# Optimization experiments

Hardware: AMD Instinct MI355X
Metric: run time of the kernel (lower is better)

The kernel has to match this reference:

```python
import jax, jax.numpy as jnp
import numpy as np

DIM = 1024


def setup_inputs() -> dict:
    key = jax.random.key(0)
    kx, kw = jax.random.split(key)
    x = jax.random.normal(kx, (4, 2048, DIM), dtype=jnp.float32)
    # fused qkv projection weight, torch Linear convention: [out_features, in_features]
    W_qkv = jax.random.normal(kw, (3 * DIM, DIM), dtype=jnp.float32) * (DIM ** -0.5)
    return {"x": x, "W_qkv": W_qkv}


def reference(x, W_qkv):
    # fused QKV projection: y = x @ W^T -> [B, N, 3*DIM]
    qkv = jnp.einsum('bnd,ed->bne', x, W_qkv)
    B, N, _ = qkv.shape
    # rearrange 'b n (e d) -> e b n d' with e=3
    qkv = qkv.reshape(B, N, 3, DIM).transpose(2, 0, 1, 3)
    q, k, v = qkv[0], qkv[1], qkv[2]
    scale = DIM ** (-0.5)  # note: scale uses full dim, module never splits heads
    attn = jnp.einsum('bnd,bmd->bnm', q * scale, k)  # [B, N, N]
    attn = jax.nn.softmax(attn, axis=-1)
    out = jnp.einsum('bnm,bmd->bnd', attn, v)
    return out
```

## Files before the change

kernel.cpp:

```cpp
#include <hip/hip_runtime.h>

using half8   = __attribute__((ext_vector_type(8))) _Float16;
using f32x4   = __attribute__((ext_vector_type(4))) float;
using ushort8 = __attribute__((ext_vector_type(8))) unsigned short;

__device__ __forceinline__ void gload16(const void* g, void* l) {
  __builtin_amdgcn_global_load_lds(
      (const __attribute__((address_space(1))) void*)g,
      (__attribute__((address_space(3))) void*)l, 16, 0, 0);
}

__device__ __forceinline__ void xcd_swizzle(int& x, int& y, int& z) {
  const int gx = gridDim.x, gy = gridDim.y;
  const int nwg = gx * gy * gridDim.z;
  const int f = blockIdx.x + gx * (blockIdx.y + gy * blockIdx.z);
  const int w = (f & 7) * (nwg >> 3) + (f >> 3);
  const int r = w >> 5, u = w & 31;
  const int nrx = gx >> 3, nry = gy >> 2;
  const int pz  = nrx * nry;
  const int rz  = r / pz, rr = r % pz;
  x = (rr % nrx) * 8 + (u & 7);
  y = (rr / nrx) * 4 + (u >> 3);
  z = rz;
}

__global__ __launch_bounds__(256) void cast_f32_f16(
    const float* __restrict__ in, unsigned short* __restrict__ out, long n) {
  long i = ((long)blockIdx.x * 256 + threadIdx.x) * 8;
  if (i >= n) return;
  float4 a = *(const float4*)(in + i);
  float4 b = *(const float4*)(in + i + 4);
  union { _Float16 h[8]; ushort8 u; } r;
  r.h[0] = (_Float16)a.x; r.h[1] = (_Float16)a.y;
  r.h[2] = (_Float16)a.z; r.h[3] = (_Float16)a.w;
  r.h[4] = (_Float16)b.x; r.h[5] = (_Float16)b.y;
  r.h[6] = (_Float16)b.z; r.h[7] = (_Float16)b.w;
  *(ushort8*)(out + i) = r.u;
}

#define FENCE_N()                                                                  \
  do {                                                                             \
    if constexpr (N_REP == 2)      asm volatile("s_waitcnt vmcnt(2)" ::: "memory");\
    else if constexpr (N_REP == 3) asm volatile("s_waitcnt vmcnt(3)" ::: "memory");\
    else                           asm volatile("s_waitcnt vmcnt(4)" ::: "memory");\
  } while (0)

#define PHASE(P, AC, AN, BC, BNX)                                                  \
  {                                                                                \
    __builtin_amdgcn_s_barrier();                                                  \
    asm volatile("s_waitcnt lgkmcnt(0)" ::: "memory");                             \
    __builtin_amdgcn_sched_barrier(0);                                             \
    __builtin_amdgcn_s_setprio(1);                                                 \
    _Pragma("unroll") for (int ks = 0; ks < 2; ++ks)                               \
    _Pragma("unroll") for (int i = 0; i < 2; ++i)                                  \
    _Pragma("unroll") for (int ni = 0; ni < N_REP; ++ni)                           \
      acc[2 * (P) + i][ni] = __builtin_amdgcn_mfma_f32_16x16x32_f16(               \
          AC[i][ks], BC[ni][ks], acc[2 * (P) + i][ni], 0, 0, 0);                   \
    __builtin_amdgcn_s_setprio(0);                                                 \
    __builtin_amdgcn_sched_barrier(0);                                             \
    if ((P) == 0 && t + 1 < nt) {                                                  \
      unsigned short* d = ldsA + (SLOT ^ 1) * ASZ + wv * 512;                      \
      const long kt = (long)(t + 1) * 64;                                          \
      gload16(aS + kt, d);                                                         \
      gload16(aS + (long)64 * lda + kt, d + 4096);                                 \
      gload16(aS + (long)128 * lda + kt, d + 8192);                                \
      gload16(aS + (long)192 * lda + kt, d + 12288);                               \
    }                                                                              \
    if ((P) == 1 && t + 2 < nt) {                                                  \
      const long kt = (long)(t + 2) * 64;                                          \
      _Pragma("unroll") for (int j = 0; j < N_REP; ++j)                            \
        gload16(bS + (long)(j * 64) * ldb + kt,                                    \
                ldsB + SLOT * BSZ + j * 4096 + wv * 512);                          \
    }                                                                              \
    if ((P) < 3) {                                                                 \
      _Pragma("unroll") for (int i = 0; i < 2; ++i) {                              \
        AN[i][0] = *(const half8*)(lA + aRd + (2 * ((P) + 1) + i) * 2048 + kg0);   \
        AN[i][1] = *(const half8*)(lA + aRd + (2 * ((P) + 1) + i) * 2048 + kg1);   \
      }                                                                            \
    } else if (t + 1 < nt) {                                                       \
      _Pragma("unroll") for (int i = 0; i < 2; ++i) {                              \
        AN[i][0] = *(const half8*)(lAo + aRd + i * 2048 + kg0);                    \
        AN[i][1] = *(const half8*)(lAo + aRd + i * 2048 + kg1);                    \
      }                                                                            \
      _Pragma("unroll") for (int ni = 0; ni < N_REP; ++ni) {                       \
        BNX[ni][0] = *(const half8*)(lBo + bRd + ni * 2048 + kg0);                 \
        BNX[ni][1] = *(const half8*)(lBo + bRd + ni * 2048 + kg1);                 \
      }                                                                            \
    }                                                                              \
    if ((P) == 2) {                                                                \
      if (t + 2 < nt) FENCE_N();                                                   \
      else asm volatile("s_waitcnt vmcnt(0)" ::: "memory");                        \
    }                                                                              \
    __builtin_amdgcn_sched_barrier(0);                                             \
  }

#define TILE(T, S, BCARR, BNARR)                                                   \
  {                                                                                \
    const int t = (T);                                                             \
    constexpr int SLOT = (S);                                                      \
    const char* lA  = (const char*)(ldsA + SLOT * ASZ);                            \
    const char* lAo = (const char*)(ldsA + (SLOT ^ 1) * ASZ);                      \
    const char* lBo = (const char*)(ldsB + (SLOT ^ 1) * BSZ);                      \
    PHASE(0, afE, afO, BCARR, BNARR)                                               \
    PHASE(1, afO, afE, BCARR, BNARR)                                               \
    PHASE(2, afE, afO, BCARR, BNARR)                                               \
    PHASE(3, afO, afE, BCARR, BNARR)                                               \
  }

template <int MODE, int N_REP>
__global__ __launch_bounds__(512, 2) void gemm8p(
    const unsigned short* __restrict__ Ab, const unsigned short* __restrict__ Bb,
    int K, int lda, int ldb, long sA, long sB,
    void* __restrict__ o0, void* __restrict__ o1, void* __restrict__ o2) {
  constexpr int BM  = 256;
  constexpr int BN  = 64 * N_REP;
  constexpr int ASZ = BM * 64;
  constexpr int BSZ = BN * 64;
  __shared__ unsigned short lds[2 * ASZ + 2 * BSZ];

  const int tid  = threadIdx.x;
  const int lane = tid & 63;
  const int wv   = tid >> 6;
  const int wr   = wv >> 2, wc = wv & 3;
  const int fr   = lane & 15, fq = lane >> 4;
  int bxi, byi, bzi;
  xcd_swizzle(bxi, byi, bzi);
  const int bm = byi * BM;
  const int bn = bxi * BN;
  const int bz = bzi;

  const unsigned short* A = Ab + (long)bz * sA;
  const unsigned short* B = Bb + (long)bz * sB;

  const int row_s = tid >> 3;
  const int col_s = ((tid & 7) ^ (row_s & 7)) * 8;
  const unsigned short* aS = A + (long)(bm + row_s) * lda + col_s;
  const unsigned short* bS = B + (long)(bn + row_s) * ldb + col_s;
  unsigned short* ldsA = lds;
  unsigned short* ldsB = lds + 2 * ASZ;

  const int kg0 = ((0 * 4 + fq) ^ (fr & 7)) * 16;
  const int kg1 = ((1 * 4 + fq) ^ (fr & 7)) * 16;
  const int aRd = (wr * 128 + fr) * 128;
  const int bRd = (wc * (16 * N_REP) + fr) * 128;

  f32x4 acc[8][N_REP] = {};
  half8 afE[2][2], afO[2][2];
  half8 bf0[N_REP][2], bf1[N_REP][2];

  const int nt = K / 64;

#pragma unroll
  for (int i = 0; i < 4; ++i)
    gload16(aS + (long)(i * 64) * lda, ldsA + i * 4096 + wv * 512);
#pragma unroll
  for (int j = 0; j < N_REP; ++j)
    gload16(bS + (long)(j * 64) * ldb, ldsB + j * 4096 + wv * 512);
  asm volatile("s_waitcnt vmcnt(0)" ::: "memory");
  __builtin_amdgcn_s_barrier();
  {
    const char* lA0 = (const char*)ldsA;
    const char* lB0 = (const char*)ldsB;
#pragma unroll
    for (int i = 0; i < 2; ++i) {
      afE[i][0] = *(const half8*)(lA0 + aRd + i * 2048 + kg0);
      afE[i][1] = *(const half8*)(lA0 + aRd + i * 2048 + kg1);
    }
#pragma unroll
    for (int ni = 0; ni < N_REP; ++ni) {
      bf0[ni][0] = *(const half8*)(lB0 + bRd + ni * 2048 + kg0);
      bf0[ni][1] = *(const half8*)(lB0 + bRd + ni * 2048 + kg1);
    }
  }
#pragma unroll
  for (int j = 0; j < N_REP; ++j)
    gload16(bS + (long)(j * 64) * ldb + 64, ldsB + BSZ + j * 4096 + wv * 512);

  for (int tt = 0; tt < nt; tt += 2) {
    TILE(tt, 0, bf0, bf1)
    TILE(tt + 1, 1, bf1, bf0)
  }

  const int row0 = bm + wr * 128 + fq * 4;
  const int col0 = bn + wc * (16 * N_REP) + fr;
#pragma unroll
  for (int mi = 0; mi < 8; ++mi) {
#pragma unroll
    for (int ni = 0; ni < N_REP; ++ni) {
      f32x4 c = acc[mi][ni];
      const long r0 = row0 + mi * 16;
      const long e  = col0 + ni * 16;
      if constexpr (MODE == 0) {
        _Float16* q  = (_Float16*)o0;
        _Float16* kk = (_Float16*)o1;
        _Float16* vv = (_Float16*)o2;
#pragma unroll
        for (int j = 0; j < 4; ++j) {
          const long i = r0 + j;
          const float val = c[j];
          if (e < 1024)      q [i * 1024 + e]          = (_Float16)(val * 0.03125f);
          else if (e < 2048) kk[i * 1024 + (e - 1024)] = (_Float16)val;
          else               vv[i * 1024 + (e - 2048)] = (_Float16)val;
        }
      } else if constexpr (MODE == 1) {
        float* C = (float*)o0 + (long)bz * 2048 * 2048;
#pragma unroll
        for (int j = 0; j < 4; ++j) C[(r0 + j) * 2048 + e] = c[j];
      } else {
        float* C = (float*)o0 + (long)bz * 2048 * 1024;
#pragma unroll
        for (int j = 0; j < 4; ++j) C[(r0 + j) * 1024 + e] = c[j];
      }
    }
  }
}

__global__ __launch_bounds__(256) void transpose_v(
    const unsigned short* __restrict__ v, unsigned short* __restrict__ vT) {
  __shared__ unsigned short t[64][72];
  const long b = blockIdx.z;
  const unsigned short* vb = v + b * (2048L * 1024);
  unsigned short* ob = vT + b * (1024L * 2048);
  const int n0 = blockIdx.y * 64;
  const int d0 = blockIdx.x * 64;
  const int tid = threadIdx.x;
  const int r  = tid >> 2;
  const int c0 = (tid & 3) * 16;
  const unsigned short* src = vb + (long)(n0 + r) * 1024 + d0 + c0;
  *(ushort4*)&t[r][c0]      = *(const ushort4*)(src);
  *(ushort4*)&t[r][c0 + 4]  = *(const ushort4*)(src + 4);
  *(ushort4*)&t[r][c0 + 8]  = *(const ushort4*)(src + 8);
  *(ushort4*)&t[r][c0 + 12] = *(const ushort4*)(src + 12);
  __syncthreads();
  union { unsigned short h[8]; ushort8 u; } w0, w1;
#pragma unroll
  for (int j = 0; j < 8; ++j) w0.h[j] = t[c0 + j][r];
#pragma unroll
  for (int j = 0; j < 8; ++j) w1.h[j] = t[c0 + 8 + j][r];
  unsigned short* dst = ob + (long)(d0 + r) * 2048 + n0 + c0;
  *(ushort8*)dst       = w0.u;
  *(ushort8*)(dst + 8) = w1.u;
}

__global__ __launch_bounds__(256) void softmax_rows(float* __restrict__ S) {
  const long row = blockIdx.x;
  float* p = S + row * 2048;
  const int t = threadIdx.x;
  float4 v0 = *(const float4*)(p + t * 8);
  float4 v1 = *(const float4*)(p + t * 8 + 4);
  float f[8] = {v0.x, v0.y, v0.z, v0.w, v1.x, v1.y, v1.z, v1.w};
  float m = f[0];
#pragma unroll
  for (int j = 1; j < 8; ++j) m = fmaxf(m, f[j]);
  for (int o = 32; o; o >>= 1) m = fmaxf(m, __shfl_xor(m, o));
  __shared__ float redm[4];
  if (!(t & 63)) redm[t >> 6] = m;
  __syncthreads();
  m = fmaxf(fmaxf(redm[0], redm[1]), fmaxf(redm[2], redm[3]));
  float e[8], s = 0.f;
#pragma unroll
  for (int j = 0; j < 8; ++j) { e[j] = __expf(f[j] - m); s += e[j]; }
  for (int o = 32; o; o >>= 1) s += __shfl_xor(s, o);
  __shared__ float reds[4];
  if (!(t & 63)) reds[t >> 6] = s;
  __syncthreads();
  s = reds[0] + reds[1] + reds[2] + reds[3];
  const float inv = 1.0f / s;
  union { _Float16 h[8]; ushort8 u; } r;
#pragma unroll
  for (int j = 0; j < 8; ++j) r.h[j] = (_Float16)(e[j] * inv);
  *(ushort8*)((unsigned short*)p + t * 8) = r.u;
}

extern "C" void kernel_launch(void* const* d_in, const int* in_sizes, int n_in,
                              void* d_out, int out_size, void* d_ws, size_t ws_size,
                              hipStream_t stream) {
  const float* x = (const float*)d_in[0];
  const float* W = (const float*)d_in[1];
  float* out = (float*)d_out;
  char* ws = (char*)d_ws;

  const long MB16 = 16777216;
  unsigned short* q  = (unsigned short*)(ws);
  unsigned short* k  = (unsigned short*)(ws + MB16);
  unsigned short* vT = (unsigned short*)(ws + 2 * MB16);
  float*          S  = (float*)(ws + 3 * MB16);
  unsigned short* xb = (unsigned short*)(ws + 3 * MB16);
  unsigned short* wb = (unsigned short*)(ws + 4 * MB16);
  unsigned short* v  = (unsigned short*)(ws + 4 * MB16 + 6291456);

  cast_f32_f16<<<4096, 256, 0, stream>>>(x, xb, 8388608L);
  cast_f32_f16<<<1536, 256, 0, stream>>>(W, wb, 3145728L);
  gemm8p<0, 3><<<dim3(16, 32, 1), 512, 0, stream>>>(
      xb, wb, 1024, 1024, 1024, 0L, 0L, q, k, v);
  transpose_v<<<dim3(16, 32, 4), 256, 0, stream>>>(v, vT);
  gemm8p<1, 2><<<dim3(16, 8, 4), 512, 0, stream>>>(
      q, k, 1024, 1024, 1024, 2048L * 1024, 2048L * 1024, S, nullptr, nullptr);
  softmax_rows<<<8192, 256, 0, stream>>>(S);
  gemm8p<2, 2><<<dim3(8, 8, 4), 512, 0, stream>>>(
      (unsigned short*)S, vT, 2048, 4096, 2048, 2048L * 4096, 1024L * 2048,
      out, nullptr, nullptr);
}
```

Measured before the change: 172.1 us.

## Restructure GEMM phase schedule to load A fragments just-in-time before barrier

Reworks the per-phase pipeline of the 8-wave GEMM. Each phase now reads its own A fragments from LDS right before the barrier and runs MFMAs after issuing the global prefetches, instead of prefetching the next phase's fragments after the MFMAs. The next tile's B fragments load in phase 3 with a partial lgkmcnt wait, and an extra barrier is added after the phase-2 vmcnt fence. The prologue also issues the second B tile before the first wait. This trades register double-buffering of A for lower register pressure but less latency hiding, and the partial waits depend on exact instruction counts.

```diff
diff --git a/kernel.cpp b/kernel.cpp
--- a/kernel.cpp
+++ b/kernel.cpp
@@ -41,24 +41,33 @@
 #define FENCE_N()                                                                  \
   do {                                                                             \
     if constexpr (N_REP == 2)      asm volatile("s_waitcnt vmcnt(2)" ::: "memory");\
-    else if constexpr (N_REP == 3) asm volatile("s_waitcnt vmcnt(3)" ::: "memory");\
-    else                           asm volatile("s_waitcnt vmcnt(4)" ::: "memory");\
+    else                           asm volatile("s_waitcnt vmcnt(3)" ::: "memory");\
   } while (0)
 
-#define PHASE(P, AC, AN, BC, BNX)                                                  \
+#define WAIT_B()                                                                   \
+  do {                                                                             \
+    if constexpr (N_REP == 2)      asm volatile("s_waitcnt lgkmcnt(4)" ::: "memory");\
+    else                           asm volatile("s_waitcnt lgkmcnt(6)" ::: "memory");\
+  } while (0)
+
+#define PHASE(P, AF, BC, BNX)                                                      \
   {                                                                                \
+    _Pragma("unroll") for (int i = 0; i < 2; ++i) {                                \
+      AF[i][0] = *(const half8*)(lA + aRd + (2 * (P) + i) * 2048 + kg0);           \
+      AF[i][1] = *(const half8*)(lA + aRd + (2 * (P) + i) * 2048 + kg1);           \
+    }                                                                              \
+    if ((P) == 3) {            \
+      _Pragma("unroll") for (int ni = 0; ni < N_REP; ++ni) {                       \
+        BNX[ni][0] = *(const half8*)(lBn + bRd + ni * 2048 + kg0);                 \
+        BNX[ni][1] = *(const half8*)(lBn + bRd + ni * 2048 + kg1);                 \
+      }                                                                            \
+    }                                                                              \
+    __builtin_amdgcn_sched_barrier(0);                                             \
     __builtin_amdgcn_s_barrier();                                                  \
-    asm volatile("s_waitcnt lgkmcnt(0)" ::: "memory");                             \
+    if ((P) == 3) WAIT_B();                                                        \
+    else asm volatile("s_waitcnt lgkmcnt(0)" ::: "memory");                        \
     __builtin_amdgcn_sched_barrier(0);                                             \
-    __builtin_amdgcn_s_setprio(1);                                                 \
-    _Pragma("unroll") for (int ks = 0; ks < 2; ++ks)                               \
-    _Pragma("unroll") for (int i = 0; i < 2; ++i)                                  \
-    _Pragma("unroll") for (int ni = 0; ni < N_REP; ++ni)                           \
-      acc[2 * (P) + i][ni] = __builtin_amdgcn_mfma_f32_16x16x32_f16(               \
-          AC[i][ks], BC[ni][ks], acc[2 * (P) + i][ni], 0, 0, 0);                   \
-    __builtin_amdgcn_s_setprio(0);                                                 \
-    __builtin_amdgcn_sched_barrier(0);                                             \
-    if ((P) == 0 && t + 1 < nt) {                                                  \
+    if ((P) == 0 && t + 1 < nt) {                          \
       unsigned short* d = ldsA + (SLOT ^ 1) * ASZ + wv * 512;                      \
       const long kt = (long)(t + 1) * 64;                                          \
       gload16(aS + kt, d);                                                         \
@@ -66,45 +75,37 @@
       gload16(aS + (long)128 * lda + kt, d + 8192);                                \
       gload16(aS + (long)192 * lda + kt, d + 12288);                               \
     }                                                                              \
-    if ((P) == 1 && t + 2 < nt) {                                                  \
+    if ((P) == 1 && t + 2 < nt) {   \
       const long kt = (long)(t + 2) * 64;                                          \
       _Pragma("unroll") for (int j = 0; j < N_REP; ++j)                            \
         gload16(bS + (long)(j * 64) * ldb + kt,                                    \
                 ldsB + SLOT * BSZ + j * 4096 + wv * 512);                          \
     }                                                                              \
-    if ((P) < 3) {                                                                 \
-      _Pragma("unroll") for (int i = 0; i < 2; ++i) {                              \
-        AN[i][0] = *(const half8*)(lA + aRd + (2 * ((P) + 1) + i) * 2048 + kg0);   \
-        AN[i][1] = *(const half8*)(lA + aRd + (2 * ((P) + 1) + i) * 2048 + kg1);   \
-      }                                                                            \
-    } else if (t + 1 < nt) {                                                       \
-      _Pragma("unroll") for (int i = 0; i < 2; ++i) {                              \
-        AN[i][0] = *(const half8*)(lAo + aRd + i * 2048 + kg0);                    \
-        AN[i][1] = *(const half8*)(lAo + aRd + i * 2048 + kg1);                    \
-      }                                                                            \
-      _Pragma("unroll") for (int ni = 0; ni < N_REP; ++ni) {                       \
-        BNX[ni][0] = *(const half8*)(lBo + bRd + ni * 2048 + kg0);                 \
-        BNX[ni][1] = *(const half8*)(lBo + bRd + ni * 2048 + kg1);                 \
-      }                                                                            \
-    }                                                                              \
+    __builtin_amdgcn_s_setprio(1);                                                 \
+    _Pragma("unroll") for (int ks = 0; ks < 2; ++ks)                               \
+    _Pragma("unroll") for (int i = 0; i < 2; ++i)                                  \
+    _Pragma("unroll") for (int ni = 0; ni < N_REP; ++ni)                           \
+      acc[2 * (P) + i][ni] = __builtin_amdgcn_mfma_f32_16x16x32_f16(               \
+          AF[i][ks], BC[ni][ks], acc[2 * (P) + i][ni], 0, 0, 0);                   \
+    __builtin_amdgcn_s_setprio(0);                                                 \
+    __builtin_amdgcn_sched_barrier(0);                                             \
     if ((P) == 2) {                                                                \
       if (t + 2 < nt) FENCE_N();                                                   \
       else asm volatile("s_waitcnt vmcnt(0)" ::: "memory");                        \
-    }                                                                              \
-    __builtin_amdgcn_sched_barrier(0);                                             \
-  }
-
-#define TILE(T, S, BCARR, BNARR)                                                   \
+      __builtin_amdgcn_s_barrier();                                                \
+    }                                                                              \
+  }
+
+#define TILE(T, S, BC, BNX)                                                        \
   {                                                                                \
     const int t = (T);                                                             \
     constexpr int SLOT = (S);                                                      \
     const char* lA  = (const char*)(ldsA + SLOT * ASZ);                            \
-    const char* lAo = (const char*)(ldsA + (SLOT ^ 1) * ASZ);                      \
-    const char* lBo = (const char*)(ldsB + (SLOT ^ 1) * BSZ);                      \
-    PHASE(0, afE, afO, BCARR, BNARR)                                               \
-    PHASE(1, afO, afE, BCARR, BNARR)                                               \
-    PHASE(2, afE, afO, BCARR, BNARR)                                               \
-    PHASE(3, afO, afE, BCARR, BNARR)                                               \
+    const char* lBn = (const char*)(ldsB + (SLOT ^ 1) * BSZ);                      \
+    PHASE(0, afA, BC, BNX)                                                         \
+    PHASE(1, afB, BC, BNX)                                                         \
+    PHASE(2, afA, BC, BNX)                                                         \
+    PHASE(3, afB, BC, BNX)                                                         \
   }
 
 template <int MODE, int N_REP>
@@ -145,7 +146,7 @@
   const int bRd = (wc * (16 * N_REP) + fr) * 128;
 
   f32x4 acc[8][N_REP] = {};
-  half8 afE[2][2], afO[2][2];
+  half8 afA[2][2], afB[2][2];
   half8 bf0[N_REP][2], bf1[N_REP][2];
 
   const int nt = K / 64;
@@ -156,25 +157,19 @@
 #pragma unroll
   for (int j = 0; j < N_REP; ++j)
     gload16(bS + (long)(j * 64) * ldb, ldsB + j * 4096 + wv * 512);
-  asm volatile("s_waitcnt vmcnt(0)" ::: "memory");
+#pragma unroll
+  for (int j = 0; j < N_REP; ++j)
+    gload16(bS + (long)(j * 64) * ldb + 64, ldsB + BSZ + j * 4096 + wv * 512);
+  FENCE_N();
   __builtin_amdgcn_s_barrier();
   {
-    const char* lA0 = (const char*)ldsA;
     const char* lB0 = (const char*)ldsB;
-#pragma unroll
-    for (int i = 0; i < 2; ++i) {
-      afE[i][0] = *(const half8*)(lA0 + aRd + i * 2048 + kg0);
-      afE[i][1] = *(const half8*)(lA0 + aRd + i * 2048 + kg1);
-    }
 #pragma unroll
     for (int ni = 0; ni < N_REP; ++ni) {
       bf0[ni][0] = *(const half8*)(lB0 + bRd + ni * 2048 + kg0);
       bf0[ni][1] = *(const half8*)(lB0 + bRd + ni * 2048 + kg1);
     }
   }
-#pragma unroll
-  for (int j = 0; j < N_REP; ++j)
-    gload16(bS + (long)(j * 64) * ldb + 64, ldsB + BSZ + j * 4096 + wv * 512);
 
   for (int tt = 0; tt < nt; tt += 2) {
     TILE(tt, 0, bf0, bf1)
```

Result: no change. 175.3 us (+1.9%).
